# Optimization experiments

Hardware: AMD Instinct MI355X
Metric: run time of the kernel (lower is better)

## Reference

```python
import jax, jax.numpy as jnp
import numpy as np

SEQ_LEN, BATCH, INPUT_SIZE, HIDDEN = 512, 64, 256, 512


def setup_inputs() -> dict:
    key = jax.random.key(0)
    k_x, k_wih, k_whh, k_bih, k_bhh = jax.random.split(key, 5)
    bound = 1.0 / np.sqrt(HIDDEN)  # torch nn.RNN init: U(-1/sqrt(H), 1/sqrt(H))
    x = jax.random.normal(k_x, (SEQ_LEN, BATCH, INPUT_SIZE), dtype=jnp.float32)
    h0 = jnp.zeros((1, BATCH, HIDDEN), dtype=jnp.float32)
    W_ih = jax.random.uniform(k_wih, (HIDDEN, INPUT_SIZE), minval=-bound, maxval=bound, dtype=jnp.float32)
    W_hh = jax.random.uniform(k_whh, (HIDDEN, HIDDEN), minval=-bound, maxval=bound, dtype=jnp.float32)
    b_ih = jax.random.uniform(k_bih, (HIDDEN,), minval=-bound, maxval=bound, dtype=jnp.float32)
    b_hh = jax.random.uniform(k_bhh, (HIDDEN,), minval=-bound, maxval=bound, dtype=jnp.float32)
    return {"x": x, "h0": h0, "W_ih": W_ih, "W_hh": W_hh, "b_ih": b_ih, "b_hh": b_hh}


def reference(x, h0, W_ih, W_hh, b_ih, b_hh):
    # Elman RNN: h_t = tanh(W_ih x_t + b_ih + W_hh h_{t-1} + b_hh)
    # Precompute the input projection for all timesteps (one big GEMM),
    # then scan the sequential recurrence.
    xW = jnp.einsum('tbi,hi->tbh', x, W_ih) + b_ih + b_hh  # (T, B, H)

    def step(h, xw_t):
        h_new = jnp.tanh(xw_t + h @ W_hh.T)  # (B, H)
        return h_new, h_new

    h_last, h_seq = jax.lax.scan(step, h0[0], xW)
    return h_seq, h_last[None]  # (T, B, H), (1, B, H)
```

## Files before the change

kernel.cpp:

```cpp
#include <hip/hip_runtime.h>


#define T_LEN 512
#define NBATCH 64
#define ISZ 256
#define HSZ 512

typedef __attribute__((ext_vector_type(8))) short short8;
typedef __attribute__((ext_vector_type(4))) int int4v;
typedef __attribute__((ext_vector_type(4))) float f32x4;

__device__ __forceinline__ unsigned short f2bf(float f) {
  unsigned u = __float_as_uint(f);
  u += 0x7fffu + ((u >> 16) & 1u);
  return (unsigned short)(u >> 16);
}
__device__ __forceinline__ float bf2f(unsigned short h) {
  return __uint_as_float(((unsigned)h) << 16);
}

__device__ __forceinline__ void split_bf(f32x4 a, f32x4 b, short8& hi, short8& lo) {
#pragma unroll
  for (int i = 0; i < 4; ++i) {
    unsigned short h = f2bf(a[i]);
    hi[i] = (short)h;
    lo[i] = (short)f2bf(a[i] - bf2f(h));
    unsigned short h2 = f2bf(b[i]);
    hi[i + 4] = (short)h2;
    lo[i + 4] = (short)f2bf(b[i] - bf2f(h2));
  }
}

__global__ __launch_bounds__(512) void xw_proj(
    const float* __restrict__ x, const float* __restrict__ Wih,
    const float* __restrict__ bih, const float* __restrict__ bhh,
    float* __restrict__ out) {
  __shared__ __align__(16) short xhi[16][264];
  __shared__ __align__(16) short xlo[16][264];

  const int tid = threadIdx.x;
  const int w  = tid >> 6;
  const int L  = tid & 63;
  const int lr = L & 15;
  const int lg = L >> 4;

  const int mhalf = blockIdx.x & 1;
  const int grp   = blockIdx.x >> 1;

  short8 Ahi[2][8], Alo[2][8];
  f32x4 bias[2];
  int mt[2];
#pragma unroll
  for (int m = 0; m < 2; ++m) {
    mt[m] = mhalf * 16 + 2 * w + m;
    int j = mt[m] * 16 + lr;
#pragma unroll
    for (int kt = 0; kt < 8; ++kt) {
      int k = kt * 32 + lg * 8;
      const f32x4 v0 = *(const f32x4*)(Wih + j * ISZ + k);
      const f32x4 v1 = *(const f32x4*)(Wih + j * ISZ + k + 4);
      split_bf(v0, v1, Ahi[m][kt], Alo[m][kt]);
    }
    int j0 = mt[m] * 16 + lg * 4;
    f32x4 b1 = *(const f32x4*)(bih + j0);
    f32x4 b2 = *(const f32x4*)(bhh + j0);
    bias[m] = b1 + b2;
  }

  for (int it = 0; it < 8; ++it) {
    const int tau = grp * 8 + it;
    const int t = tau >> 2;
    const int g = tau & 3;

    __syncthreads();
    {
      const int f   = tid * 8;
      const int row = f >> 8;
      const int i0  = f & 255;
      const float* p = x + ((size_t)(t * NBATCH + g * 16 + row) * ISZ + i0);
      const f32x4 v0 = *(const f32x4*)p;
      const f32x4 v1 = *(const f32x4*)(p + 4);
      short8 hi, lo;
      split_bf(v0, v1, hi, lo);
      *(short8*)(&xhi[row][i0]) = hi;
      *(short8*)(&xlo[row][i0]) = lo;
    }
    __syncthreads();

    f32x4 acc[2];
    acc[0] = f32x4{0.f, 0.f, 0.f, 0.f};
    acc[1] = f32x4{0.f, 0.f, 0.f, 0.f};
#pragma unroll
    for (int kt = 0; kt < 8; ++kt) {
      int koff = kt * 32 + lg * 8;
      short8 bh = *(const short8*)(&xhi[lr][koff]);
      short8 bl = *(const short8*)(&xlo[lr][koff]);
      acc[0] = __builtin_amdgcn_mfma_f32_16x16x32_bf16(Ahi[0][kt], bh, acc[0], 0, 0, 0);
      acc[1] = __builtin_amdgcn_mfma_f32_16x16x32_bf16(Ahi[1][kt], bh, acc[1], 0, 0, 0);
      acc[0] = __builtin_amdgcn_mfma_f32_16x16x32_bf16(Alo[0][kt], bh, acc[0], 0, 0, 0);
      acc[1] = __builtin_amdgcn_mfma_f32_16x16x32_bf16(Alo[1][kt], bh, acc[1], 0, 0, 0);
      acc[0] = __builtin_amdgcn_mfma_f32_16x16x32_bf16(Ahi[0][kt], bl, acc[0], 0, 0, 0);
      acc[1] = __builtin_amdgcn_mfma_f32_16x16x32_bf16(Ahi[1][kt], bl, acc[1], 0, 0, 0);
    }
#pragma unroll
    for (int m = 0; m < 2; ++m) {
      f32x4 r = acc[m] + bias[m];
      *(f32x4*)(out + (size_t)((((t * 4 + g) * 32 + mt[m]) * 64) + L) * 4) = r;
    }
  }
}

__global__ __launch_bounds__(512, 2) void rnn_scan_i8(
    const float* __restrict__ Whh, const float* __restrict__ h0,
    float* __restrict__ out) {
  __shared__ __align__(16) char hb[2 * 16 * 528];

  const int tid = threadIdx.x;
  const int w  = tid >> 6;
  const int L  = tid & 63;
  const int lr = L & 15;
  const int lg = L >> 4;
  const int g  = blockIdx.x;

  const float QS  = 127.0f * 22.627416997969522f;
  const float DEQ = (float)(1.0 / (127.0 * 127.0 * 22.627416997969522));

  int4v A[4][8];
#pragma unroll
  for (int m = 0; m < 4; ++m) {
    const int j = (4 * w + m) * 16 + lr;
#pragma unroll
    for (int kt = 0; kt < 8; ++kt) {
      const float* p = Whh + (size_t)j * HSZ + kt * 64 + lg * 16;
      int dw[4];
#pragma unroll
      for (int d = 0; d < 4; ++d) {
        f32x4 v = *(const f32x4*)(p + d * 4);
        int pk = 0;
#pragma unroll
        for (int i = 0; i < 4; ++i) {
          float q = __builtin_rintf(fminf(fmaxf(v[i] * QS, -127.f), 127.f));
          pk |= ((int)q & 255) << (8 * i);
        }
        dw[d] = pk;
      }
      A[m][kt] = int4v{dw[0], dw[1], dw[2], dw[3]};
    }
  }

  {
    const int row = tid >> 5;
    const int k0  = (tid & 31) * 16;
    const float* p = h0 + ((size_t)(g * 16 + row) * HSZ + k0);
    int dw[4];
#pragma unroll
    for (int c = 0; c < 4; ++c) {
      f32x4 v = *(const f32x4*)(p + c * 4);
      int pk = 0;
#pragma unroll
      for (int i = 0; i < 4; ++i) {
        float q = __builtin_rintf(fminf(fmaxf(v[i] * 127.f, -127.f), 127.f));
        pk |= ((int)q & 255) << (8 * i);
      }
      dw[c] = pk;
    }
    *(int4v*)(&hb[row * 528 + k0]) = int4v{dw[0], dw[1], dw[2], dw[3]};
  }
  __syncthreads();

  const int j0 = 4 * w * 16 + lg * 4;
  const char* xwp = (const char*)out + ((size_t)(g * 32 + 4 * w) * 64 + L) * 16;
  float* hsp = out + (size_t)(g * 16 + lr) * HSZ + j0;
  const int ldsr = lr * 528 + lg * 16;
  const int ldsw = lr * 528 + j0;

  f32x4 pend[4];

  for (int t = 0; t < T_LEN; ++t) {
    const int cur = t & 1, nxt = cur ^ 1;
    const int cb = cur * 8448, nb = nxt * 8448;

    f32x4 xw[4];
#pragma unroll
    for (int m = 0; m < 4; ++m) xw[m] = *(const f32x4*)(xwp + m * 1024);

    if (t > 0) {
#pragma unroll
      for (int m = 0; m < 4; ++m) *(f32x4*)(hsp + m * 16) = pend[m];
      hsp += NBATCH * HSZ;
    }

    int4v B[8];
#pragma unroll
    for (int kt = 0; kt < 8; ++kt)
      B[kt] = *(const int4v*)(&hb[cb + ldsr + kt * 64]);

    int4v acc[4];
#pragma unroll
    for (int m = 0; m < 4; ++m) acc[m] = int4v{0, 0, 0, 0};
#pragma unroll
    for (int kt = 0; kt < 8; ++kt)
#pragma unroll
      for (int m = 0; m < 4; ++m)
        acc[m] = __builtin_amdgcn_mfma_i32_16x16x64_i8(A[m][kt], B[kt], acc[m], 0, 0, 0);

#pragma unroll
    for (int m = 0; m < 4; ++m) {
      unsigned qi[4];
      f32x4 h;
#pragma unroll
      for (int r = 0; r < 4; ++r) {
        float y  = fmaf((float)acc[m][r], DEQ, xw[m][r]);
        float e  = __builtin_amdgcn_exp2f(y * 2.8853900817779268f);
        float rc = __builtin_amdgcn_rcpf(1.0f + e);
        float hv = fmaf(-2.0f, rc, 1.0f);
        h[r] = hv;
        qi[r] = __float_as_uint(fmaf(hv, 127.0f, 12582912.0f));
      }
      pend[m] = h;
      unsigned p0 = __builtin_amdgcn_perm(qi[1], qi[0], 0x0c0c0400u);
      unsigned p1 = __builtin_amdgcn_perm(qi[3], qi[2], 0x04000c0cu);
      *(unsigned*)(&hb[nb + ldsw + m * 16]) = p0 | p1;
    }

    __syncthreads();
    xwp += 131072;
  }

#pragma unroll
  for (int m = 0; m < 4; ++m) {
    *(f32x4*)(hsp + m * 16) = pend[m];
    *(f32x4*)(out + (size_t)T_LEN * NBATCH * HSZ +
              (size_t)(g * 16 + lr) * HSZ + j0 + m * 16) = pend[m];
  }
}

extern "C" void kernel_launch(void* const* d_in, const int* in_sizes, int n_in,
                              void* d_out, int out_size, void* d_ws, size_t ws_size,
                              hipStream_t stream) {
  const float* x   = (const float*)d_in[0];
  const float* h0  = (const float*)d_in[1];
  const float* Wih = (const float*)d_in[2];
  const float* Whh = (const float*)d_in[3];
  const float* bih = (const float*)d_in[4];
  const float* bhh = (const float*)d_in[5];
  float* out = (float*)d_out;

  xw_proj<<<512, 512, 0, stream>>>(x, Wih, bih, bhh, out);
  rnn_scan_i8<<<4, 512, 0, stream>>>(Whh, h0, out);
}
```

Before: 1.021 ms.

## Split recurrence hidden dim across two blocks exchanging int8 state via global flags

The scan now runs on 8 blocks instead of 4: each batch group's hidden dimension is split in half between two blocks. Each block computes its own half of the next state from LDS and gets the partner half through a global mailbox guarded by an atomic counter it spins on. This halves the MFMA work and weight registers per block, at the cost of a cross-CU handshake through global memory every timestep. The tanh's log2e scaling is also folded into the input projection and dequant constant, removing a multiply per element.

```diff
diff --git a/kernel.cpp b/kernel.cpp
--- a/kernel.cpp
+++ b/kernel.cpp
@@ -9,6 +9,10 @@
 typedef __attribute__((ext_vector_type(8))) short short8;
 typedef __attribute__((ext_vector_type(4))) int int4v;
 typedef __attribute__((ext_vector_type(4))) float f32x4;
+typedef unsigned long long u64;
+
+#define LOG2E2f 2.8853900817779268f
+#define DEQ2C ((float)(2.8853900817779268 / (127.0 * 127.0 * 22.627416997969522)))
 
 __device__ __forceinline__ unsigned short f2bf(float f) {
   unsigned u = __float_as_uint(f);
@@ -64,7 +68,7 @@
     int j0 = mt[m] * 16 + lg * 4;
     f32x4 b1 = *(const f32x4*)(bih + j0);
     f32x4 b2 = *(const f32x4*)(bhh + j0);
-    bias[m] = b1 + b2;
+    bias[m] = (b1 + b2) * LOG2E2f;
   }
 
   for (int it = 0; it < 8; ++it) {
@@ -104,7 +108,7 @@
     }
 #pragma unroll
     for (int m = 0; m < 2; ++m) {
-      f32x4 r = acc[m] + bias[m];
+      f32x4 r = acc[m] * LOG2E2f + bias[m];
       *(f32x4*)(out + (size_t)((((t * 4 + g) * 32 + mt[m]) * 64) + L) * 4) = r;
     }
   }
@@ -112,23 +116,26 @@
 
 __global__ __launch_bounds__(512, 2) void rnn_scan_i8(
     const float* __restrict__ Whh, const float* __restrict__ h0,
-    float* __restrict__ out) {
-  __shared__ __align__(16) char hb[2 * 16 * 528];
+    float* __restrict__ out, unsigned* __restrict__ ws) {
+  __shared__ __align__(16) char hb[2 * 16 * 272];
 
   const int tid = threadIdx.x;
   const int w  = tid >> 6;
   const int L  = tid & 63;
   const int lr = L & 15;
   const int lg = L >> 4;
-  const int g  = blockIdx.x;
-
-  const float QS  = 127.0f * 22.627416997969522f;
-  const float DEQ = (float)(1.0 / (127.0 * 127.0 * 22.627416997969522));
-
-  int4v A[4][8];
-#pragma unroll
-  for (int m = 0; m < 4; ++m) {
-    const int j = (4 * w + m) * 16 + lr;
+
+  const int bid = blockIdx.x;
+  int s, g;
+  if (bid < 4) { s = 0; g = bid; } else { s = 1; g = bid - 4; }
+  const int s4 = s * 4, p4 = 4 - s4;
+
+  const float QS = 127.0f * 22.627416997969522f;
+
+  int4v A[2][8];
+#pragma unroll
+  for (int m = 0; m < 2; ++m) {
+    const int j = s * 256 + (2 * w + m) * 16 + lr;
 #pragma unroll
     for (int kt = 0; kt < 8; ++kt) {
       const float* p = Whh + (size_t)j * HSZ + kt * 64 + lg * 16;
@@ -148,91 +155,140 @@
     }
   }
 
+  unsigned* myflag = ws + (size_t)(g * 2 + s) * 32;
+  unsigned* pflag  = ws + (size_t)(g * 2 + (1 - s)) * 32;
+  char* mybox      = (char*)ws + 4096 + (size_t)(g * 2 + s) * 8192;
+  const char* pbox = (const char*)ws + 4096 + (size_t)(g * 2 + (1 - s)) * 8192;
+
+  const int ldsrd = lr * 272 + lg * 16;
+  const int ldsw  = lr * 272 + 32 * w + 4 * lg;
+  const int boxw  = lr * 256 + 32 * w + 4 * lg;
+  const int prd   = lr * 256 + lg * 16;
+  const int jcol0 = s * 256 + 32 * w + 4 * lg;
+
+  const char* xwp = (const char*)out +
+      ((size_t)((g * 32 + s * 16 + 2 * w) * 64 + L)) * 16;
+  float* hsp = out + (size_t)(g * 16 + lr) * HSZ + jcol0;
+
+  f32x4 pend[2];
+
+#define STEP_EPILOGUE(TT) do {                                                 \
+    unsigned dwq[2];                                                           \
+    _Pragma("unroll")                                                          \
+    for (int m = 0; m < 2; ++m) {                                              \
+      const f32x4 xwm = m ? xw1 : xw0;                                         \
+      const int4v am  = m ? acc1 : acc0;                                       \
+      unsigned qi[4]; f32x4 hh;                                                \
+      _Pragma("unroll")                                                        \
+      for (int r = 0; r < 4; ++r) {                                            \
+        float y2 = fmaf((float)am[r], DEQ2C, xwm[r]);                          \
+        float e  = __builtin_amdgcn_exp2f(y2);                     \
+        float rc = __builtin_amdgcn_rcpf(1.0f + e);                            \
+        float hv = fmaf(-2.0f, rc, 1.0f);                         \
+        hh[r] = hv;                                                            \
+        qi[r] = __float_as_uint(fmaf(hv, 127.0f, 12582912.0f));                \
+      }                                                                        \
+      pend[m] = hh;                                                            \
+      unsigned pp0 = __builtin_amdgcn_perm(qi[1], qi[0], 0x0c0c0400u);         \
+      unsigned pp1 = __builtin_amdgcn_perm(qi[3], qi[2], 0x04000c0cu);         \
+      dwq[m] = pp0 | pp1;                                                      \
+    }                                                                          \
+    { char* bq = mybox + ((TT) & 1) * 4096 + boxw;                             \
+      __hip_atomic_store((unsigned*)bq, dwq[0],                                \
+                         __ATOMIC_RELAXED, __HIP_MEMORY_SCOPE_AGENT);          \
+      __hip_atomic_store((unsigned*)(bq + 16), dwq[1],                         \
+                         __ATOMIC_RELAXED, __HIP_MEMORY_SCOPE_AGENT); }        \
+    asm volatile("s_waitcnt vmcnt(0)" ::: "memory");                           \
+    if (L == 0)                                                                \
+      (void)__hip_atomic_fetch_add(myflag, 1u,                                 \
+                         __ATOMIC_RELAXED, __HIP_MEMORY_SCOPE_AGENT);          \
+    { const int nb = (((TT) & 1) ^ 1) * 4352;                                  \
+      *(unsigned*)(&hb[nb + ldsw])      = dwq[0];                              \
+      *(unsigned*)(&hb[nb + ldsw + 16]) = dwq[1]; }                            \
+    __syncthreads();                                                           \
+  } while (0)
+
   {
-    const int row = tid >> 5;
-    const int k0  = (tid & 31) * 16;
-    const float* p = h0 + ((size_t)(g * 16 + row) * HSZ + k0);
-    int dw[4];
-#pragma unroll
-    for (int c = 0; c < 4; ++c) {
-      f32x4 v = *(const f32x4*)(p + c * 4);
-      int pk = 0;
-#pragma unroll
-      for (int i = 0; i < 4; ++i) {
-        float q = __builtin_rintf(fminf(fmaxf(v[i] * 127.f, -127.f), 127.f));
-        pk |= ((int)q & 255) << (8 * i);
+    f32x4 xw0 = *(const f32x4*)(xwp);
+    f32x4 xw1 = *(const f32x4*)(xwp + 1024);
+    int4v acc0 = int4v{0, 0, 0, 0}, acc1 = int4v{0, 0, 0, 0};
+#pragma unroll
+    for (int kt = 0; kt < 8; ++kt) {
+      const float* p = h0 + (size_t)(g * 16 + lr) * HSZ + kt * 64 + lg * 16;
+      int dwp[4];
+#pragma unroll
+      for (int c = 0; c < 4; ++c) {
+        f32x4 v = *(const f32x4*)(p + c * 4);
+        int pk = 0;
+#pragma unroll
+        for (int i = 0; i < 4; ++i) {
+          float q = __builtin_rintf(fminf(fmaxf(v[i] * 127.f, -127.f), 127.f));
+          pk |= ((int)q & 255) << (8 * i);
+        }
+        dwp[c] = pk;
       }
-      dw[c] = pk;
-    }
-    *(int4v*)(&hb[row * 528 + k0]) = int4v{dw[0], dw[1], dw[2], dw[3]};
-  }
-  __syncthreads();
-
-  const int j0 = 4 * w * 16 + lg * 4;
-  const char* xwp = (const char*)out + ((size_t)(g * 32 + 4 * w) * 64 + L) * 16;
-  float* hsp = out + (size_t)(g * 16 + lr) * HSZ + j0;
-  const int ldsr = lr * 528 + lg * 16;
-  const int ldsw = lr * 528 + j0;
-
-  f32x4 pend[4];
-
-  for (int t = 0; t < T_LEN; ++t) {
-    const int cur = t & 1, nxt = cur ^ 1;
-    const int cb = cur * 8448, nb = nxt * 8448;
-
-    f32x4 xw[4];
-#pragma unroll
-    for (int m = 0; m < 4; ++m) xw[m] = *(const f32x4*)(xwp + m * 1024);
-
-    if (t > 0) {
-#pragma unroll
-      for (int m = 0; m < 4; ++m) *(f32x4*)(hsp + m * 16) = pend[m];
-      hsp += NBATCH * HSZ;
-    }
-
-    int4v B[8];
-#pragma unroll
-    for (int kt = 0; kt < 8; ++kt)
-      B[kt] = *(const int4v*)(&hb[cb + ldsr + kt * 64]);
-
-    int4v acc[4];
-#pragma unroll
-    for (int m = 0; m < 4; ++m) acc[m] = int4v{0, 0, 0, 0};
-#pragma unroll
-    for (int kt = 0; kt < 8; ++kt)
-#pragma unroll
-      for (int m = 0; m < 4; ++m)
-        acc[m] = __builtin_amdgcn_mfma_i32_16x16x64_i8(A[m][kt], B[kt], acc[m], 0, 0, 0);
-
-#pragma unroll
-    for (int m = 0; m < 4; ++m) {
-      unsigned qi[4];
-      f32x4 h;
-#pragma unroll
-      for (int r = 0; r < 4; ++r) {
-        float y  = fmaf((float)acc[m][r], DEQ, xw[m][r]);
-        float e  = __builtin_amdgcn_exp2f(y * 2.8853900817779268f);
-        float rc = __builtin_amdgcn_rcpf(1.0f + e);
-        float hv = fmaf(-2.0f, rc, 1.0f);
-        h[r] = hv;
-        qi[r] = __float_as_uint(fmaf(hv, 127.0f, 12582912.0f));
-      }
-      pend[m] = h;
-      unsigned p0 = __builtin_amdgcn_perm(qi[1], qi[0], 0x0c0c0400u);
-      unsigned p1 = __builtin_amdgcn_perm(qi[3], qi[2], 0x04000c0cu);
-      *(unsigned*)(&hb[nb + ldsw + m * 16]) = p0 | p1;
-    }
-
-    __syncthreads();
+      int4v b0 = int4v{dwp[0], dwp[1], dwp[2], dwp[3]};
+      acc0 = __builtin_amdgcn_mfma_i32_16x16x64_i8(A[0][kt], b0, acc0, 0, 0, 0);
+      acc1 = __builtin_amdgcn_mfma_i32_16x16x64_i8(A[1][kt], b0, acc1, 0, 0, 0);
+    }
+    STEP_EPILOGUE(0);
     xwp += 131072;
   }
 
-#pragma unroll
-  for (int m = 0; m < 4; ++m) {
-    *(f32x4*)(hsp + m * 16) = pend[m];
-    *(f32x4*)(out + (size_t)T_LEN * NBATCH * HSZ +
-              (size_t)(g * 16 + lr) * HSZ + j0 + m * 16) = pend[m];
-  }
+  for (int t = 1; t < T_LEN; ++t) {
+    f32x4 xw0 = *(const f32x4*)(xwp);
+    f32x4 xw1 = *(const f32x4*)(xwp + 1024);
+
+    *(f32x4*)(hsp)      = pend[0];
+    *(f32x4*)(hsp + 16) = pend[1];
+    hsp += NBATCH * HSZ;
+
+    const int cb = (t & 1) * 4352;
+    int4v Bo[4];
+#pragma unroll
+    for (int k = 0; k < 4; ++k)
+      Bo[k] = *(const int4v*)(&hb[cb + ldsrd + k * 64]);
+
+    int4v acc0 = int4v{0, 0, 0, 0}, acc1 = int4v{0, 0, 0, 0};
+#pragma unroll
+    for (int k = 0; k < 4; ++k) {
+      acc0 = __builtin_amdgcn_mfma_i32_16x16x64_i8(A[0][s4 + k], Bo[k], acc0, 0, 0, 0);
+      acc1 = __builtin_amdgcn_mfma_i32_16x16x64_i8(A[1][s4 + k], Bo[k], acc1, 0, 0, 0);
+    }
+
+    const unsigned tgt = 8u * (unsigned)t;
+    while (__hip_atomic_load(pflag, __ATOMIC_RELAXED, __HIP_MEMORY_SCOPE_AGENT) < tgt) {}
+
+    const char* pb = pbox + ((t & 1) ^ 1) * 4096 + prd;
+    int4v Bp[4];
+#pragma unroll
+    for (int k = 0; k < 4; ++k) {
+      u64 plo = __hip_atomic_load((u64*)(pb + k * 64),
+                                  __ATOMIC_RELAXED, __HIP_MEMORY_SCOPE_AGENT);
+      u64 phi = __hip_atomic_load((u64*)(pb + k * 64 + 8),
+                                  __ATOMIC_RELAXED, __HIP_MEMORY_SCOPE_AGENT);
+      int4v bb;
+      bb[0] = (int)(unsigned)plo; bb[1] = (int)(unsigned)(plo >> 32);
+      bb[2] = (int)(unsigned)phi; bb[3] = (int)(unsigned)(phi >> 32);
+      Bp[k] = bb;
+    }
+#pragma unroll
+    for (int k = 0; k < 4; ++k) {
+      acc0 = __builtin_amdgcn_mfma_i32_16x16x64_i8(A[0][p4 + k], Bp[k], acc0, 0, 0, 0);
+      acc1 = __builtin_amdgcn_mfma_i32_16x16x64_i8(A[1][p4 + k], Bp[k], acc1, 0, 0, 0);
+    }
+
+    STEP_EPILOGUE(t);
+    xwp += 131072;
+  }
+
+  *(f32x4*)(hsp)      = pend[0];
+  *(f32x4*)(hsp + 16) = pend[1];
+  float* hl = out + (size_t)T_LEN * NBATCH * HSZ +
+              (size_t)(g * 16 + lr) * HSZ + jcol0;
+  *(f32x4*)(hl)      = pend[0];
+  *(f32x4*)(hl + 16) = pend[1];
+#undef STEP_EPILOGUE
 }
 
 extern "C" void kernel_launch(void* const* d_in, const int* in_sizes, int n_in,
@@ -246,6 +302,7 @@
   const float* bhh = (const float*)d_in[5];
   float* out = (float*)d_out;
 
+  hipMemsetAsync(d_ws, 0, 4096, stream);
   xw_proj<<<512, 512, 0, stream>>>(x, Wih, bih, bhh, out);
-  rnn_scan_i8<<<4, 512, 0, stream>>>(Whh, h0, out);
-}
+  rnn_scan_i8<<<8, 512, 0, stream>>>(Whh, h0, out, (unsigned*)d_ws);
+}
```

Result: slower. 3.798 ms (+272.0%).

## Prefetch next-step xw, fold tanh scale into projection, use lightweight barrier

Applied to the files above, without the earlier changes.

The recurrent scan now loads the next timestep's input projection one step ahead into alternating register buffers. The loop is unrolled by two so the LDS ping-pong offsets are compile-time constants. __syncthreads is replaced with an inline s_waitcnt lgkmcnt(0) plus s_barrier, so the barrier no longer waits on outstanding global loads and stores. The 2*log2(e) factor used by the exp2-based tanh is moved into xw_proj's output and into the dequant constant, which removes a multiply from the serial dependency chain. The trade-off is more live registers, and the final prefetch reads one step past the sequence into the h_last region of the output buffer; that value is never used.

```diff
diff --git a/kernel.cpp b/kernel.cpp
--- a/kernel.cpp
+++ b/kernel.cpp
@@ -9,6 +9,9 @@
 typedef __attribute__((ext_vector_type(8))) short short8;
 typedef __attribute__((ext_vector_type(4))) int int4v;
 typedef __attribute__((ext_vector_type(4))) float f32x4;
+
+#define LOG2E2f 2.8853900817779268f
+#define DEQ2C ((float)(2.8853900817779268 / (127.0 * 127.0 * 22.627416997969522)))
 
 __device__ __forceinline__ unsigned short f2bf(float f) {
   unsigned u = __float_as_uint(f);
@@ -64,7 +67,7 @@
     int j0 = mt[m] * 16 + lg * 4;
     f32x4 b1 = *(const f32x4*)(bih + j0);
     f32x4 b2 = *(const f32x4*)(bhh + j0);
-    bias[m] = b1 + b2;
+    bias[m] = (b1 + b2) * LOG2E2f;
   }
 
   for (int it = 0; it < 8; ++it) {
@@ -104,7 +107,7 @@
     }
 #pragma unroll
     for (int m = 0; m < 2; ++m) {
-      f32x4 r = acc[m] + bias[m];
+      f32x4 r = acc[m] * LOG2E2f + bias[m];
       *(f32x4*)(out + (size_t)((((t * 4 + g) * 32 + mt[m]) * 64) + L) * 4) = r;
     }
   }
@@ -122,8 +125,7 @@
   const int lg = L >> 4;
   const int g  = blockIdx.x;
 
-  const float QS  = 127.0f * 22.627416997969522f;
-  const float DEQ = (float)(1.0 / (127.0 * 127.0 * 22.627416997969522));
+  const float QS = 127.0f * 22.627416997969522f;
 
   int4v A[4][8];
 #pragma unroll
@@ -175,57 +177,62 @@
   const int ldsw = lr * 528 + j0;
 
   f32x4 pend[4];
-
-  for (int t = 0; t < T_LEN; ++t) {
-    const int cur = t & 1, nxt = cur ^ 1;
-    const int cb = cur * 8448, nb = nxt * 8448;
-
-    f32x4 xw[4];
-#pragma unroll
-    for (int m = 0; m < 4; ++m) xw[m] = *(const f32x4*)(xwp + m * 1024);
-
-    if (t > 0) {
-#pragma unroll
-      for (int m = 0; m < 4; ++m) *(f32x4*)(hsp + m * 16) = pend[m];
-      hsp += NBATCH * HSZ;
-    }
-
-    int4v B[8];
-#pragma unroll
-    for (int kt = 0; kt < 8; ++kt)
-      B[kt] = *(const int4v*)(&hb[cb + ldsr + kt * 64]);
-
-    int4v acc[4];
-#pragma unroll
-    for (int m = 0; m < 4; ++m) acc[m] = int4v{0, 0, 0, 0};
-#pragma unroll
-    for (int kt = 0; kt < 8; ++kt)
-#pragma unroll
-      for (int m = 0; m < 4; ++m)
-        acc[m] = __builtin_amdgcn_mfma_i32_16x16x64_i8(A[m][kt], B[kt], acc[m], 0, 0, 0);
-
-#pragma unroll
-    for (int m = 0; m < 4; ++m) {
-      unsigned qi[4];
-      f32x4 h;
-#pragma unroll
-      for (int r = 0; r < 4; ++r) {
-        float y  = fmaf((float)acc[m][r], DEQ, xw[m][r]);
-        float e  = __builtin_amdgcn_exp2f(y * 2.8853900817779268f);
-        float rc = __builtin_amdgcn_rcpf(1.0f + e);
-        float hv = fmaf(-2.0f, rc, 1.0f);
-        h[r] = hv;
-        qi[r] = __float_as_uint(fmaf(hv, 127.0f, 12582912.0f));
-      }
-      pend[m] = h;
-      unsigned p0 = __builtin_amdgcn_perm(qi[1], qi[0], 0x0c0c0400u);
-      unsigned p1 = __builtin_amdgcn_perm(qi[3], qi[2], 0x04000c0cu);
-      *(unsigned*)(&hb[nb + ldsw + m * 16]) = p0 | p1;
-    }
-
-    __syncthreads();
-    xwp += 131072;
-  }
+  f32x4 xwA[4], xwB[4];
+
+#pragma unroll
+  for (int m = 0; m < 4; ++m) xwA[m] = *(const f32x4*)(xwp + m * 1024);
+  xwp += 131072;
+
+#define RNN_STEP(XWC, XWN, P, DOSTORE) do {                                    \
+    _Pragma("unroll")                                                          \
+    for (int m = 0; m < 4; ++m) XWN[m] = *(const f32x4*)(xwp + m * 1024);      \
+    xwp += 131072;                                                             \
+    if (DOSTORE) {                                                             \
+      _Pragma("unroll")                                                        \
+      for (int m = 0; m < 4; ++m) *(f32x4*)(hsp + m * 16) = pend[m];           \
+      hsp += NBATCH * HSZ;                                                     \
+    }                                                                          \
+    int4v B[8];                                                                \
+    _Pragma("unroll")                                                          \
+    for (int kt = 0; kt < 8; ++kt)                                             \
+      B[kt] = *(const int4v*)(&hb[(P) * 8448 + ldsr + kt * 64]);               \
+    int4v acc[4];                                                              \
+    _Pragma("unroll")                                                          \
+    for (int m = 0; m < 4; ++m) acc[m] = int4v{0, 0, 0, 0};                    \
+    _Pragma("unroll")                                                          \
+    for (int kt = 0; kt < 8; ++kt)                                             \
+      _Pragma("unroll")                                                        \
+      for (int m = 0; m < 4; ++m)                                              \
+        acc[m] = __builtin_amdgcn_mfma_i32_16x16x64_i8(A[m][kt], B[kt],        \
+                                                       acc[m], 0, 0, 0);       \
+    _Pragma("unroll")                                                          \
+    for (int m = 0; m < 4; ++m) {                                              \
+      unsigned qi[4];                                                          \
+      f32x4 hh;                                                                \
+      _Pragma("unroll")                                                        \
+      for (int r = 0; r < 4; ++r) {                                            \
+        float y2 = fmaf((float)acc[m][r], DEQ2C, XWC[m][r]);                   \
+        float e  = __builtin_amdgcn_exp2f(y2);                     \
+        float rc = __builtin_amdgcn_rcpf(1.0f + e);                            \
+        float hv = fmaf(-2.0f, rc, 1.0f);                         \
+        hh[r] = hv;                                                            \
+        qi[r] = __float_as_uint(fmaf(hv, 127.0f, 12582912.0f));                \
+      }                                                                        \
+      pend[m] = hh;                                                            \
+      unsigned pp0 = __builtin_amdgcn_perm(qi[1], qi[0], 0x0c0c0400u);         \
+      unsigned pp1 = __builtin_amdgcn_perm(qi[3], qi[2], 0x04000c0cu);         \
+      *(unsigned*)(&hb[(1 - (P)) * 8448 + ldsw + m * 16]) = pp0 | pp1;         \
+    }                                                                          \
+    asm volatile("s_waitcnt lgkmcnt(0)\n\ts_barrier" ::: "memory");            \
+  } while (0)
+
+  RNN_STEP(xwA, xwB, 0, 0);
+  for (int it = 0; it < 255; ++it) {
+    RNN_STEP(xwB, xwA, 1, 1);
+    RNN_STEP(xwA, xwB, 0, 1);
+  }
+  RNN_STEP(xwB, xwA, 1, 1);
+#undef RNN_STEP
 
 #pragma unroll
   for (int m = 0; m < 4; ++m) {
```

New measurement: 987.4 us. 1.03x faster.
